# Kernel optimization log

Measured on AMD Instinct MI355X. Metric: run time of the kernel, lower is better.

## Reference

```python
import jax, jax.numpy as jnp
import numpy as np

B, N, D, C, H, W = 4, 900, 256, 256, 200, 200
HEADS, LVLS, PTS, K = 8, 1, 4, 10


def setup_inputs() -> dict:
    key = jax.random.key(0)
    ks = jax.random.split(key, 16)
    s = 0.02
    return {
        "query_embed": jax.random.normal(ks[0], (B, N, D), jnp.float32),
        "ctrl_points": jax.random.uniform(ks[1], (B, N, 4, 2), jnp.float32, -50.0, 50.0),
        "bev_features": jax.random.normal(ks[2], (B, C, H, W), jnp.float32),
        "spatial_shapes": jnp.array([[H, W]], dtype=jnp.int32),
        "pc_range": jnp.array([-51.2, -51.2, -5.0, 51.2, 51.2, 3.0], jnp.float32),
        "Wq": s * jax.random.normal(ks[3], (D, D)), "bq": jnp.zeros((D,)),
        "Wv": s * jax.random.normal(ks[4], (C, D)), "bv": jnp.zeros((D,)),
        "Woff": s * jax.random.normal(ks[5], (D, HEADS * LVLS * PTS * 2)), "boff": jnp.zeros((HEADS * LVLS * PTS * 2,)),
        "Wattn": s * jax.random.normal(ks[6], (D, HEADS * LVLS * PTS)), "battn": jnp.zeros((HEADS * LVLS * PTS,)),
        "Wmo": s * jax.random.normal(ks[7], (D, D)), "bmo": jnp.zeros((D,)),
        "Wo": s * jax.random.normal(ks[8], (D, D)), "bo": jnp.zeros((D,)),
    }


def _forward(query_embed, ctrl_points, bev_features, spatial_shapes, pc_range,
             Wq, bq, Wv, bv, Woff, boff, Wattn, battn, Wmo, bmo, Wo, bo):
    b, n, d = query_embed.shape
    _, c, h, w = bev_features.shape
    hd = d // HEADS

    # --- cubic Bezier interpolation: (B,N,4,2) -> (B,N,K,2) dense points ---
    t = jnp.linspace(0.0, 1.0, K, dtype=query_embed.dtype)
    basis = jnp.stack([(1 - t) ** 3, 3 * (1 - t) ** 2 * t, 3 * (1 - t) * t ** 2, t ** 3], axis=-1)  # (K,4)
    dense = jnp.einsum('kc,bncd->bnkd', basis, ctrl_points)
    # --- normalize to [0,1] by pc_range, clamp to [0.01,0.99] ---
    nx = (dense[..., 0] - pc_range[0]) / (pc_range[3] - pc_range[0])
    ny = (dense[..., 1] - pc_range[1]) / (pc_range[4] - pc_range[1])
    ref = jnp.clip(jnp.stack([nx, ny], axis=-1), 0.01, 0.99)  # (B,N,K,2)

    # --- projections ---
    q = query_embed @ Wq + bq                                       # (B,N,D) (identity for residual)
    v = bev_features.reshape(b, c, h * w).transpose(0, 2, 1) @ Wv + bv  # (B,HW,D)
    v = v.reshape(b, h * w, HEADS, hd)

    off = (q @ Woff + boff).reshape(b, n, HEADS, LVLS, PTS, 2)
    aw = jax.nn.softmax((q @ Wattn + battn).reshape(b, n, HEADS, LVLS * PTS), axis=-1)
    aw = aw.reshape(b, n, HEADS, PTS)  # LVLS == 1

    # offset normalizer = (W, H) per level
    normalizer = jnp.stack([spatial_shapes[..., 1], spatial_shapes[..., 0]], axis=-1).astype(q.dtype)  # (L,2)
    # sampling locations: broadcast K bezier points against heads/points offsets
    loc = ref[:, :, None, :, None, :] + off / normalizer[None, None, None, :, None, :]  # (B,N,HEADS,K,PTS,2)

    # --- bilinear sampling, align_corners=False, zero padding ---
    gx = loc[..., 0] * w - 0.5
    gy = loc[..., 1] * h - 0.5
    x0 = jnp.floor(gx)
    y0 = jnp.floor(gy)
    wx = gx - x0
    wy = gy - y0
    x0i = x0.astype(jnp.int32)
    y0i = y0.astype(jnp.int32)

    vflat = v.transpose(0, 2, 1, 3).reshape(b * HEADS, h * w, hd)  # (B*HEADS, HW, hd)

    def flat(a):  # (B,N,HEADS,K,PTS) -> (B*HEADS, N*K*PTS)
        return a.transpose(0, 2, 1, 3, 4).reshape(b * HEADS, n * K * PTS)

    acc = jnp.zeros((b * HEADS, n * K * PTS, hd), dtype=q.dtype)
    for dx, dy in ((0, 0), (1, 0), (0, 1), (1, 1)):
        ix = flat(x0i) + dx
        iy = flat(y0i) + dy
        wxx = flat(wx) if dx else (1.0 - flat(wx))
        wyy = flat(wy) if dy else (1.0 - flat(wy))
        valid = (ix >= 0) & (ix < w) & (iy >= 0) & (iy < h)
        idx = jnp.clip(iy, 0, h - 1) * w + jnp.clip(ix, 0, w - 1)
        corner = jnp.take_along_axis(vflat, idx[..., None], axis=1)  # (B*HEADS, Npts, hd)
        acc = acc + corner * (wxx * wyy * valid.astype(q.dtype))[..., None]

    sampled = acc.reshape(b, HEADS, n, K, PTS, hd)
    # weighted sum over (K, PTS); attention weights shared across the K bezier points
    out = jnp.einsum('bhnkpd,bnhp->bnhd', sampled, aw).reshape(b, n, d)
    out = out @ Wmo + bmo + q   # mmcv MSDeformAttn output_proj + residual (identity = query)
    out = out @ Wo + bo         # outer output_proj
    return out


def reference(query_embed, ctrl_points, bev_features, spatial_shapes, pc_range,
              Wq, bq, Wv, bv, Woff, boff, Wattn, battn, Wmo, bmo, Wo, bo):
    return _forward(query_embed, ctrl_points, bev_features, spatial_shapes, pc_range,
                    Wq, bq, Wv, bv, Woff, boff, Wattn, battn, Wmo, bmo, Wo, bo)
```

## Files before the change

kernel.cpp:

```cpp
#include <hip/hip_runtime.h>
#include <hip/hip_bf16.h>
#include <math.h>


typedef unsigned short u16;
typedef unsigned int u32;
typedef short bf16x8 __attribute__((ext_vector_type(8)));
typedef float f32x4 __attribute__((ext_vector_type(4)));

__device__ __forceinline__ float bf2f(u16 u) {
  union { u32 i; float f; } c; c.i = ((u32)u) << 16; return c.f;
}
__device__ __forceinline__ u16 f2bf(float f) {
  union { float f; u32 i; } c; c.f = f;
  u32 u = c.i;
  return (u16)((u + 0x7FFFu + ((u >> 16) & 1u)) >> 16);
}
__device__ __forceinline__ int imin(int a, int b) { return a < b ? a : b; }
__device__ __forceinline__ int imax(int a, int b) { return a > b ? a : b; }

__device__ __forceinline__ void glds16(const u16* g, u16* l) {
  __builtin_amdgcn_global_load_lds(
      (__attribute__((address_space(1))) const void*)g,
      (__attribute__((address_space(3))) void*)l, 16, 0, 0);
}

__global__ __launch_bounds__(256) void prep_weights(
    const float* __restrict__ Wq, const float* __restrict__ Wv,
    const float* __restrict__ Woff, const float* __restrict__ Wattn,
    const float* __restrict__ Wmo, const float* __restrict__ Wo,
    const float* __restrict__ boff, const float* __restrict__ battn,
    const float* __restrict__ query,
    u16* __restrict__ wqT, u16* __restrict__ wvT, u16* __restrict__ woaT,
    u16* __restrict__ wmoT, u16* __restrict__ woT, float* __restrict__ boa,
    u16* __restrict__ qin)
{
  int idx = blockIdx.x * 256 + threadIdx.x;
  {
    int i = idx * 4;
    float4 v = *(const float4*)(query + i);
    uint2 st;
    st.x = (u32)f2bf(v.x) | ((u32)f2bf(v.y) << 16);
    st.y = (u32)f2bf(v.z) | ((u32)f2bf(v.w) << 16);
    *(uint2*)(qin + i) = st;
  }
  if (idx < 65536) {
    int r = idx >> 8, c = idx & 255;
    wqT[idx]  = f2bf(Wq[c * 256 + r]);
    wvT[idx]  = f2bf(Wv[c * 256 + r]);
    wmoT[idx] = f2bf(Wmo[c * 256 + r]);
    woT[idx]  = f2bf(Wo[c * 256 + r]);
  }
  if (idx < 96 * 256) {
    int n = idx >> 8, k = idx & 255;
    woaT[idx] = f2bf((n < 64) ? Woff[k * 64 + n] : Wattn[k * 32 + (n - 64)]);
  }
  if (idx < 96) boa[idx] = (idx < 64) ? boff[idx] : battn[idx - 64];
}

__global__ __launch_bounds__(256) void transpose_bev(
    const float* __restrict__ bev, u16* __restrict__ bevT)
{
  __shared__ u16 t[64 * 66];
  const int b = blockIdx.z, c0 = blockIdx.y * 64, p0 = blockIdx.x * 64;
  const float* src = bev + ((size_t)b * 256 + c0) * 40000 + p0;
#pragma unroll
  for (int it = 0; it < 4; ++it) {
    int slot = it * 256 + threadIdx.x;
    int r = slot >> 4, i = slot & 15;
    float4 dv = *(const float4*)(src + (size_t)r * 40000 + i * 4);
    u32* dst = (u32*)&t[r * 66 + i * 4];
    dst[0] = (u32)f2bf(dv.x) | ((u32)f2bf(dv.y) << 16);
    dst[1] = (u32)f2bf(dv.z) | ((u32)f2bf(dv.w) << 16);
  }
  __syncthreads();
  u16* ob = bevT + ((size_t)b * 40000 + p0) * 256 + c0;
#pragma unroll
  for (int it = 0; it < 2; ++it) {
    int slot = it * 256 + threadIdx.x;
    int pr = slot >> 3, ci = slot & 7;
    u32 w0 = (u32)t[(ci * 8 + 0) * 66 + pr] | ((u32)t[(ci * 8 + 1) * 66 + pr] << 16);
    u32 w1 = (u32)t[(ci * 8 + 2) * 66 + pr] | ((u32)t[(ci * 8 + 3) * 66 + pr] << 16);
    u32 w2 = (u32)t[(ci * 8 + 4) * 66 + pr] | ((u32)t[(ci * 8 + 5) * 66 + pr] << 16);
    u32 w3 = (u32)t[(ci * 8 + 6) * 66 + pr] | ((u32)t[(ci * 8 + 7) * 66 + pr] << 16);
    uint4 ov; ov.x = w0; ov.y = w1; ov.z = w2; ov.w = w3;
    *(uint4*)(ob + (size_t)pr * 256 + ci * 8) = ov;
  }
}

enum { GM_F32 = 0, GM_BF16 = 1, GM_BOTH = 2, GM_V = 3 };

template <int MODE, bool HAS_RES>
__global__ __launch_bounds__(256) void gemm_bt(
    const u16* __restrict__ A, const u16* __restrict__ Bt,
    const float* __restrict__ bias, const float* __restrict__ res,
    u16* __restrict__ outb, float* __restrict__ outf,
    int M, int N, int K, long long btStrideZ, long long outStrideZ)
{
  __shared__ __align__(16) u16 lA[128 * 32];
  __shared__ __align__(16) u16 lB[128 * 32];
  const int tid = threadIdx.x;
  const int wv = tid >> 6, lane = tid & 63;
  const int m0 = blockIdx.y * 128, n0 = blockIdx.x * 128;
  const u16* Bz = Bt + (size_t)blockIdx.z * btStrideZ;

  const int crow = lane >> 2;
  const int ckoff = (lane & 3) * 8;
  const int a1 = imin(m0 + wv * 16 + crow, M - 1);
  const int a2 = imin(m0 + (wv + 4) * 16 + crow, M - 1);
  const int b1 = imin(n0 + wv * 16 + crow, N - 1);
  const int b2 = imin(n0 + (wv + 4) * 16 + crow, N - 1);
  const u16* gA1 = A + (size_t)a1 * K + ckoff;
  const u16* gA2 = A + (size_t)a2 * K + ckoff;
  const u16* gB1 = Bz + (size_t)b1 * K + ckoff;
  const u16* gB2 = Bz + (size_t)b2 * K + ckoff;
  u16* lA1 = lA + wv * 512;  u16* lA2 = lA + (wv + 4) * 512;
  u16* lB1 = lB + wv * 512;  u16* lB2 = lB + (wv + 4) * 512;

  const int fm = (wv & 1) * 64, fn = (wv >> 1) * 64;
  const int fr = lane & 15, fk = (lane >> 4) * 8;

  f32x4 acc[4][4];
#pragma unroll
  for (int i = 0; i < 4; ++i)
#pragma unroll
    for (int j = 0; j < 4; ++j) acc[i][j] = (f32x4){0.f, 0.f, 0.f, 0.f};

  for (int k0 = 0; k0 < K; k0 += 32) {
    glds16(gA1 + k0, lA1);
    glds16(gA2 + k0, lA2);
    glds16(gB1 + k0, lB1);
    glds16(gB2 + k0, lB2);
    __syncthreads();
    bf16x8 af[4], bfv[4];
#pragma unroll
    for (int i = 0; i < 4; ++i)
      af[i] = *(const bf16x8*)&lA[(fm + i * 16 + fr) * 32 + fk];
#pragma unroll
    for (int j = 0; j < 4; ++j)
      bfv[j] = *(const bf16x8*)&lB[(fn + j * 16 + fr) * 32 + fk];
    __syncthreads();
#pragma unroll
    for (int i = 0; i < 4; ++i)
#pragma unroll
      for (int j = 0; j < 4; ++j)
        acc[i][j] = __builtin_amdgcn_mfma_f32_16x16x32_bf16(af[i], bfv[j], acc[i][j], 0, 0, 0);
  }

  const int quad = lane >> 4;
#pragma unroll
  for (int j = 0; j < 4; ++j) {
    const int n = n0 + fn + j * 16 + fr;
    const bool nok = (n < N);
    float bcol = 0.f;
    if (MODE != GM_V) bcol = bias[nok ? n : 0];
#pragma unroll
    for (int i = 0; i < 4; ++i) {
      const int mb = m0 + fm + i * 16 + quad * 4;
      if (MODE == GM_V) {
        if (nok) {
          u16 u0 = f2bf(acc[i][j][0] + bias[mb + 0]);
          u16 u1 = f2bf(acc[i][j][1] + bias[mb + 1]);
          u16 u2 = f2bf(acc[i][j][2] + bias[mb + 2]);
          u16 u3 = f2bf(acc[i][j][3] + bias[mb + 3]);
          size_t off = (size_t)blockIdx.z * outStrideZ +
                       (size_t)(mb >> 5) * (40000 * 32) + (size_t)n * 32 + (mb & 31);
          uint2 st; st.x = (u32)u0 | ((u32)u1 << 16); st.y = (u32)u2 | ((u32)u3 << 16);
          *(uint2*)(outb + off) = st;
        }
      } else {
#pragma unroll
        for (int r = 0; r < 4; ++r) {
          const int m = mb + r;
          if (m < M && nok) {
            float x = acc[i][j][r] + bcol;
            if (HAS_RES) x += res[(size_t)m * N + n];
            if (MODE == GM_F32) outf[(size_t)m * N + n] = x;
            else if (MODE == GM_BF16) outb[(size_t)m * N + n] = f2bf(x);
            else { outb[(size_t)m * N + n] = f2bf(x); outf[(size_t)m * N + n] = x; }
          }
        }
      }
    }
  }
}

__global__ __launch_bounds__(256) void sampler(
    const float* __restrict__ ctrl,
    const float* __restrict__ pc,
    const float* __restrict__ oa_,
    const u16* __restrict__ v,
    u16* __restrict__ attn_out)
{
  __shared__ int   sX0[4][40], sY0[4][40];
  __shared__ float sWx[4][40], sWy[4][40], sAw[4][40];
  const int w = threadIdx.x >> 6, lane = threadIdx.x & 63;
  const int bh = blockIdx.x & 31;
  const int n = (blockIdx.x >> 5) * 4 + w;
  const int h = bh & 7, b = bh >> 3;
  const int row = b * 900 + n;

  if (lane < 40) {
    const int k = lane >> 2, p = lane & 3;
    const float t = (float)k * (1.0f / 9.0f), u = 1.f - t;
    const float c0 = u * u * u, c1 = 3.f * u * u * t, c2 = 3.f * u * t * t, c3 = t * t * t;
    const float* cp = ctrl + (size_t)row * 8;
    float cx = c0 * cp[0] + c1 * cp[2] + c2 * cp[4] + c3 * cp[6];
    float cy = c0 * cp[1] + c1 * cp[3] + c2 * cp[5] + c3 * cp[7];
    float nx = (cx - pc[0]) / (pc[3] - pc[0]);
    float ny = (cy - pc[1]) / (pc[4] - pc[1]);
    nx = fminf(fmaxf(nx, 0.01f), 0.99f);
    ny = fminf(fmaxf(ny, 0.01f), 0.99f);
    const float* oa = oa_ + (size_t)row * 96;
    float ox = oa[h * 8 + p * 2 + 0], oy = oa[h * 8 + p * 2 + 1];
    float l0 = oa[64 + h * 4 + 0], l1 = oa[64 + h * 4 + 1];
    float l2 = oa[64 + h * 4 + 2], l3 = oa[64 + h * 4 + 3];
    float mx = fmaxf(fmaxf(l0, l1), fmaxf(l2, l3));
    float e0 = __expf(l0 - mx), e1 = __expf(l1 - mx), e2 = __expf(l2 - mx), e3 = __expf(l3 - mx);
    float lp = (p == 0) ? l0 : (p == 1) ? l1 : (p == 2) ? l2 : l3;
    float aw = __expf(lp - mx) / (e0 + e1 + e2 + e3);
    float gx = (nx + ox * (1.f / 200.f)) * 200.f - 0.5f;
    float gy = (ny + oy * (1.f / 200.f)) * 200.f - 0.5f;
    float x0 = floorf(gx), y0 = floorf(gy);
    sX0[w][lane] = (int)x0; sY0[w][lane] = (int)y0;
    sWx[w][lane] = gx - x0; sWy[w][lane] = gy - y0; sAw[w][lane] = aw;
  }
  __syncthreads();

  const int sub = lane >> 5, ch = lane & 31;
  const u16* vb = v + ((size_t)(b * 8 + h)) * (40000 * 32) + ch;
  float acc = 0.f;
#pragma unroll 4
  for (int i = 0; i < 20; ++i) {
    const int s = sub * 20 + i;
    const int x0 = sX0[w][s], y0 = sY0[w][s];
    const float wx = sWx[w][s], wy = sWy[w][s], aw = sAw[w][s];
    const int x1 = x0 + 1, y1 = y0 + 1;
    const int cx0 = imin(imax(x0, 0), 199), cx1 = imin(imax(x1, 0), 199);
    const int cy0 = imin(imax(y0, 0), 199), cy1 = imin(imax(y1, 0), 199);
    const bool vx0 = (u32)x0 < 200u, vx1 = (u32)x1 < 200u;
    const bool vy0 = (u32)y0 < 200u, vy1 = (u32)y1 < 200u;
    const u16* r0 = vb + (size_t)(cy0 * 200) * 32;
    const u16* r1 = vb + (size_t)(cy1 * 200) * 32;
    float f00 = bf2f(r0[cx0 * 32]);
    float f10 = bf2f(r0[cx1 * 32]);
    float f01 = bf2f(r1[cx0 * 32]);
    float f11 = bf2f(r1[cx1 * 32]);
    float w00 = (vx0 && vy0) ? (1.f - wx) * (1.f - wy) : 0.f;
    float w10 = (vx1 && vy0) ? wx * (1.f - wy) : 0.f;
    float w01 = (vx0 && vy1) ? (1.f - wx) * wy : 0.f;
    float w11 = (vx1 && vy1) ? wx * wy : 0.f;
    acc += aw * (w00 * f00 + w10 * f10 + w01 * f01 + w11 * f11);
  }
  acc += __shfl_down(acc, 32);
  if (lane < 32) attn_out[(size_t)row * 256 + h * 32 + ch] = f2bf(acc);
}

extern "C" void kernel_launch(void* const* d_in, const int* in_sizes, int n_in,
                              void* d_out, int out_size, void* d_ws, size_t ws_size,
                              hipStream_t stream)
{
  const float* query = (const float*)d_in[0];
  const float* ctrl  = (const float*)d_in[1];
  const float* bev   = (const float*)d_in[2];
  const float* pc    = (const float*)d_in[4];
  const float* Wq    = (const float*)d_in[5];  const float* bq    = (const float*)d_in[6];
  const float* Wv    = (const float*)d_in[7];  const float* bv    = (const float*)d_in[8];
  const float* Woff  = (const float*)d_in[9];  const float* boff  = (const float*)d_in[10];
  const float* Wattn = (const float*)d_in[11]; const float* battn = (const float*)d_in[12];
  const float* Wmo   = (const float*)d_in[13]; const float* bmo   = (const float*)d_in[14];
  const float* Wo    = (const float*)d_in[15]; const float* bo    = (const float*)d_in[16];

  char* ws = (char*)d_ws;
  size_t off = 0;
  auto alloc = [&](size_t bytes) -> void* {
    void* p = ws + off; off += (bytes + 255) & ~(size_t)255; return p;
  };
  u16*  bevT = (u16*)alloc(4ull * 40000 * 256 * 2);
  u16*  v    = (u16*)alloc(4ull * 8 * 40000 * 32 * 2);
  u16*  qin  = (u16*)alloc(3600ull * 256 * 2);
  u16*  wqT  = (u16*)alloc(65536 * 2);
  u16*  wvT  = (u16*)alloc(65536 * 2);
  u16*  woaT = (u16*)alloc(96 * 256 * 2);
  u16*  wmoT = (u16*)alloc(65536 * 2);
  u16*  woT  = (u16*)alloc(65536 * 2);
  float* boa = (float*)alloc(96 * 4);
  float* qf  = (float*)alloc(3600ull * 256 * 4);
  u16*  qb   = (u16*)alloc(3600ull * 256 * 2);
  float* oaf = (float*)alloc(3600ull * 96 * 4);
  u16*  atnO = (u16*)alloc(3600ull * 256 * 2);
  u16*  out1 = (u16*)alloc(3600ull * 256 * 2);
  (void)ws_size; (void)in_sizes; (void)n_in; (void)out_size;

  prep_weights<<<900, 256, 0, stream>>>(Wq, Wv, Woff, Wattn, Wmo, Wo, boff, battn,
                                        query, wqT, wvT, woaT, wmoT, woT, boa, qin);
  transpose_bev<<<dim3(625, 4, 4), 256, 0, stream>>>(bev, bevT);
  gemm_bt<GM_BOTH, false><<<dim3(2, 29, 1), 256, 0, stream>>>(
      qin, wqT, bq, nullptr, qb, qf, 3600, 256, 256, 0, 0);
  gemm_bt<GM_F32, false><<<dim3(1, 29, 1), 256, 0, stream>>>(
      qb, woaT, boa, nullptr, nullptr, oaf, 3600, 96, 256, 0, 0);
  gemm_bt<GM_V, false><<<dim3(313, 2, 4), 256, 0, stream>>>(
      wvT, bevT, bv, nullptr, v, nullptr, 256, 40000, 256,
      40000ll * 256, 8ll * 40000 * 32);
  sampler<<<7200, 256, 0, stream>>>(ctrl, pc, oaf, v, atnO);
  gemm_bt<GM_BF16, true><<<dim3(2, 29, 1), 256, 0, stream>>>(
      atnO, wmoT, bmo, qf, out1, nullptr, 3600, 256, 256, 0, 0);
  gemm_bt<GM_F32, false><<<dim3(2, 29, 1), 256, 0, stream>>>(
      out1, woT, bo, nullptr, nullptr, (float*)d_out, 3600, 256, 256, 0, 0);
}
```

Measured before the change: 432.9 us.

## Vectorize sampler corner loads across channels and swap V-GEMM grid order

The sampler now has each lane load 4 bf16 channels (8 bytes) per bilinear corner, with 8 sample groups per wave. Partial sums are reduced with xor shuffles and written as a packed 8-byte store. The attention weight is folded into the corner weights. The value-projection GEMM also swaps its block x/y mapping so the two M-tiles sharing a B tile run next to each other, which should improve cache reuse of bevT. The cost is a longer shuffle reduction and more registers per lane.

```diff
diff --git a/kernel.cpp b/kernel.cpp
--- a/kernel.cpp
+++ b/kernel.cpp
@@ -10,6 +10,12 @@
 
 __device__ __forceinline__ float bf2f(u16 u) {
   union { u32 i; float f; } c; c.i = ((u32)u) << 16; return c.f;
+}
+__device__ __forceinline__ float bflo(u32 w) {
+  union { u32 i; float f; } c; c.i = w << 16; return c.f;
+}
+__device__ __forceinline__ float bfhi(u32 w) {
+  union { u32 i; float f; } c; c.i = w & 0xffff0000u; return c.f;
 }
 __device__ __forceinline__ u16 f2bf(float f) {
   union { float f; u32 i; } c; c.f = f;
@@ -90,7 +96,7 @@
 
 enum { GM_F32 = 0, GM_BF16 = 1, GM_BOTH = 2, GM_V = 3 };
 
-template <int MODE, bool HAS_RES>
+template <int MODE, bool HAS_RES, bool XY_SWAP>
 __global__ __launch_bounds__(256) void gemm_bt(
     const u16* __restrict__ A, const u16* __restrict__ Bt,
     const float* __restrict__ bias, const float* __restrict__ res,
@@ -101,7 +107,8 @@
   __shared__ __align__(16) u16 lB[128 * 32];
   const int tid = threadIdx.x;
   const int wv = tid >> 6, lane = tid & 63;
-  const int m0 = blockIdx.y * 128, n0 = blockIdx.x * 128;
+  const int m0 = (XY_SWAP ? blockIdx.x : blockIdx.y) * 128;
+  const int n0 = (XY_SWAP ? blockIdx.y : blockIdx.x) * 128;
   const u16* Bz = Bt + (size_t)blockIdx.z * btStrideZ;
 
   const int crow = lane >> 2;
@@ -227,12 +234,13 @@
   }
   __syncthreads();
 
-  const int sub = lane >> 5, ch = lane & 31;
-  const u16* vb = v + ((size_t)(b * 8 + h)) * (40000 * 32) + ch;
-  float acc = 0.f;
-#pragma unroll 4
-  for (int i = 0; i < 20; ++i) {
-    const int s = sub * 20 + i;
+  const int sg = lane >> 3;
+  const int ch0 = (lane & 7) * 4;
+  const u16* vb = v + ((size_t)(b * 8 + h)) * (40000 * 32) + ch0;
+  float a0 = 0.f, a1 = 0.f, a2 = 0.f, a3 = 0.f;
+#pragma unroll
+  for (int p = 0; p < 5; ++p) {
+    const int s = p * 8 + sg;
     const int x0 = sX0[w][s], y0 = sY0[w][s];
     const float wx = sWx[w][s], wy = sWy[w][s], aw = sAw[w][s];
     const int x1 = x0 + 1, y1 = y0 + 1;
@@ -240,20 +248,32 @@
     const int cy0 = imin(imax(y0, 0), 199), cy1 = imin(imax(y1, 0), 199);
     const bool vx0 = (u32)x0 < 200u, vx1 = (u32)x1 < 200u;
     const bool vy0 = (u32)y0 < 200u, vy1 = (u32)y1 < 200u;
-    const u16* r0 = vb + (size_t)(cy0 * 200) * 32;
-    const u16* r1 = vb + (size_t)(cy1 * 200) * 32;
-    float f00 = bf2f(r0[cx0 * 32]);
-    float f10 = bf2f(r0[cx1 * 32]);
-    float f01 = bf2f(r1[cx0 * 32]);
-    float f11 = bf2f(r1[cx1 * 32]);
-    float w00 = (vx0 && vy0) ? (1.f - wx) * (1.f - wy) : 0.f;
-    float w10 = (vx1 && vy0) ? wx * (1.f - wy) : 0.f;
-    float w01 = (vx0 && vy1) ? (1.f - wx) * wy : 0.f;
-    float w11 = (vx1 && vy1) ? wx * wy : 0.f;
-    acc += aw * (w00 * f00 + w10 * f10 + w01 * f01 + w11 * f11);
-  }
-  acc += __shfl_down(acc, 32);
-  if (lane < 32) attn_out[(size_t)row * 256 + h * 32 + ch] = f2bf(acc);
+    const float w00 = (vx0 && vy0) ? aw * (1.f - wx) * (1.f - wy) : 0.f;
+    const float w10 = (vx1 && vy0) ? aw * wx * (1.f - wy) : 0.f;
+    const float w01 = (vx0 && vy1) ? aw * (1.f - wx) * wy : 0.f;
+    const float w11 = (vx1 && vy1) ? aw * wx * wy : 0.f;
+    uint2 d00 = *(const uint2*)(vb + (size_t)(cy0 * 200 + cx0) * 32);
+    uint2 d10 = *(const uint2*)(vb + (size_t)(cy0 * 200 + cx1) * 32);
+    uint2 d01 = *(const uint2*)(vb + (size_t)(cy1 * 200 + cx0) * 32);
+    uint2 d11 = *(const uint2*)(vb + (size_t)(cy1 * 200 + cx1) * 32);
+    a0 += w00 * bflo(d00.x) + w10 * bflo(d10.x) + w01 * bflo(d01.x) + w11 * bflo(d11.x);
+    a1 += w00 * bfhi(d00.x) + w10 * bfhi(d10.x) + w01 * bfhi(d01.x) + w11 * bfhi(d11.x);
+    a2 += w00 * bflo(d00.y) + w10 * bflo(d10.y) + w01 * bflo(d01.y) + w11 * bflo(d11.y);
+    a3 += w00 * bfhi(d00.y) + w10 * bfhi(d10.y) + w01 * bfhi(d01.y) + w11 * bfhi(d11.y);
+  }
+#pragma unroll
+  for (int off = 8; off < 64; off <<= 1) {
+    a0 += __shfl_xor(a0, off);
+    a1 += __shfl_xor(a1, off);
+    a2 += __shfl_xor(a2, off);
+    a3 += __shfl_xor(a3, off);
+  }
+  if (lane < 8) {
+    uint2 st;
+    st.x = (u32)f2bf(a0) | ((u32)f2bf(a1) << 16);
+    st.y = (u32)f2bf(a2) | ((u32)f2bf(a3) << 16);
+    *(uint2*)(attn_out + (size_t)row * 256 + h * 32 + ch0) = st;
+  }
 }
 
 extern "C" void kernel_launch(void* const* d_in, const int* in_sizes, int n_in,
@@ -295,16 +315,16 @@
   prep_weights<<<900, 256, 0, stream>>>(Wq, Wv, Woff, Wattn, Wmo, Wo, boff, battn,
                                         query, wqT, wvT, woaT, wmoT, woT, boa, qin);
   transpose_bev<<<dim3(625, 4, 4), 256, 0, stream>>>(bev, bevT);
-  gemm_bt<GM_BOTH, false><<<dim3(2, 29, 1), 256, 0, stream>>>(
+  gemm_bt<GM_BOTH, false, false><<<dim3(2, 29, 1), 256, 0, stream>>>(
       qin, wqT, bq, nullptr, qb, qf, 3600, 256, 256, 0, 0);
-  gemm_bt<GM_F32, false><<<dim3(1, 29, 1), 256, 0, stream>>>(
+  gemm_bt<GM_F32, false, false><<<dim3(1, 29, 1), 256, 0, stream>>>(
       qb, woaT, boa, nullptr, nullptr, oaf, 3600, 96, 256, 0, 0);
-  gemm_bt<GM_V, false><<<dim3(313, 2, 4), 256, 0, stream>>>(
+  gemm_bt<GM_V, false, true><<<dim3(2, 313, 4), 256, 0, stream>>>(
       wvT, bevT, bv, nullptr, v, nullptr, 256, 40000, 256,
       40000ll * 256, 8ll * 40000 * 32);
   sampler<<<7200, 256, 0, stream>>>(ctrl, pc, oaf, v, atnO);
-  gemm_bt<GM_BF16, true><<<dim3(2, 29, 1), 256, 0, stream>>>(
+  gemm_bt<GM_BF16, true, false><<<dim3(2, 29, 1), 256, 0, stream>>>(
       atnO, wmoT, bmo, qf, out1, nullptr, 3600, 256, 256, 0, 0);
-  gemm_bt<GM_F32, false><<<dim3(2, 29, 1), 256, 0, stream>>>(
+  gemm_bt<GM_F32, false, false><<<dim3(2, 29, 1), 256, 0, stream>>>(
       out1, woT, bo, nullptr, nullptr, (float*)d_out, 3600, 256, 256, 0, 0);
 }
```

Measured after the change: 419.3 us. 1.03x faster.
